# Performance work log

Measured on AMD Instinct MI355X. Metric: run time of the kernel, lower is better.

Reference implementation:

```python
import jax, jax.numpy as jnp
import numpy as np

# ---------- spherical offset pattern (setup-time, numpy, exact port) ----------

def _get_xy(dp, dt):
    t, c = np.tan, np.cos
    return np.array([
        [(-t(dt), 1/c(dt)*t(dp)), (0, t(dp)), (t(dt), 1/c(dt)*t(dp))],
        [(-t(dt), 0),             (1, 1),     (t(dt), 0)],
        [(-t(dt), -1/c(dt)*t(dp)), (0, -t(dp)), (t(dt), -1/c(dt)*t(dp))]])


def _cal_offset(h, w, r, c):
    phi = -((r + 0.5) / h * np.pi - np.pi / 2)
    theta = (c + 0.5) / w * 2 * np.pi - np.pi
    xys = _get_xy(np.pi / h, 2 * np.pi / w)
    x, y = xys[..., 0], xys[..., 1]
    rho = np.sqrt(x ** 2 + y ** 2)
    v = np.arctan(rho)
    new_phi = np.arcsin(np.cos(v) * np.sin(phi) + y * np.sin(v) * np.cos(phi) / rho)
    new_theta = theta + np.arctan(x * np.sin(v) / (rho * np.cos(phi) * np.cos(v) - y * np.sin(phi) * np.sin(v)))
    new_r = (-new_phi + np.pi / 2) * h / np.pi - 0.5
    new_c = (new_theta + np.pi) * w / 2 / np.pi - 0.5
    new_c = (new_c + w) % w
    res = np.stack([new_r, new_c], axis=-1)
    res[1, 1] = (r, c)
    for i in range(3):
        for j in range(3):
            res[i, j, 0] -= (r + i - 1)
            res[i, j, 1] -= (c + j - 1)
    return res.reshape(-1)  # (18,) ordered k=i*3+j, pairs (dy, dx)


def _offsets_map(h, w):
    with np.errstate(all='ignore'):
        co = np.array([[_cal_offset(h, w, i, j) for j in range(w)] for i in range(h)])
    return co.transpose(2, 0, 1)  # (18, h, w)


# ---------- jax forward ----------

def _bilinear_gather(x, py, px):
    # x: [B,C,H,W]; py/px: [K,H,W] float sample coords. Zero padding outside.
    B, C, H, W = x.shape
    y0 = jnp.floor(py); x0 = jnp.floor(px)
    wy = py - y0; wx = px - x0
    y0i = y0.astype(jnp.int32); x0i = x0.astype(jnp.int32)
    xf = x.reshape(B, C, H * W)

    def corner(yi, xi, wgt):
        valid = (yi >= 0) & (yi < H) & (xi >= 0) & (xi < W)
        idx = (jnp.clip(yi, 0, H - 1) * W + jnp.clip(xi, 0, W - 1)).reshape(-1)
        v = jnp.take(xf, idx, axis=2).reshape(B, C, *py.shape)  # [B,C,K,H,W]
        return v * (wgt * valid.astype(x.dtype))[None, None]

    return (corner(y0i,     x0i,     (1 - wy) * (1 - wx)) +
            corner(y0i,     x0i + 1, (1 - wy) * wx) +
            corner(y0i + 1, x0i,     wy * (1 - wx)) +
            corner(y0i + 1, x0i + 1, wy * wx))


def _forward(x, weight, bias, w_down, w_up, scale, offset):
    B, C, H, W = x.shape
    O = weight.shape[0]
    # frozen dense 3x3 conv (stride 1, pad 1)
    h = jax.lax.conv_general_dilated(
        x, weight, window_strides=(1, 1), padding=((1, 1), (1, 1)),
        dimension_numbers=('NCHW', 'OIHW', 'NCHW'))
    h = h + bias[None, :, None, None]
    # deform_conv2d with fixed spherical offsets (offset: [18,H,W] -> [9,2,H,W])
    off = offset.reshape(9, 2, H, W)
    dy, dx_ = off[:, 0], off[:, 1]
    kk = jnp.arange(9)
    ki = (kk // 3).astype(x.dtype); kj = (kk % 3).astype(x.dtype)
    pp = jnp.arange(H, dtype=x.dtype); qq = jnp.arange(W, dtype=x.dtype)
    py = pp[None, :, None] - 1.0 + ki[:, None, None] + dy  # [9,H,W]
    px = qq[None, None, :] - 1.0 + kj[:, None, None] + dx_
    sampled = _bilinear_gather(x, py, px)                   # [B,C,9,H,W]
    dconv = jnp.einsum('bckhw,ock->bohw', sampled, weight.reshape(O, C, 9))
    dconv = dconv + bias[None, :, None, None]
    # concat + dual 1x1 conv LoRA fusion + scaled residual
    cat = jnp.concatenate([dconv, h], axis=1)               # [B,2O,H,W]
    down = jnp.einsum('bchw,oc->bohw', cat, w_down)
    up = jnp.einsum('bchw,oc->bohw', down, w_up)
    return h + scale * up


def setup_inputs() -> dict:
    key = jax.random.key(0)
    ks = jax.random.split(key, 6)
    B, C, O, H, W = 4, 320, 320, 64, 64
    low = max(O // 1, 1)
    x = jax.random.normal(ks[0], (B, C, H, W), dtype=jnp.float32)
    weight = jax.random.normal(ks[1], (O, C, 3, 3), dtype=jnp.float32) * 0.02
    bias = jax.random.normal(ks[2], (O,), dtype=jnp.float32) * 0.02
    w_down = jax.random.normal(ks[3], (low, 2 * O), dtype=jnp.float32) * 0.02
    w_up = jax.random.normal(ks[4], (O, low), dtype=jnp.float32) * 0.02
    scale = jnp.asarray(1.0, dtype=jnp.float32)
    offset = jnp.asarray(_offsets_map(H, W), dtype=jnp.float32)  # [18,H,W]
    return {'x': x, 'weight': weight, 'bias': bias, 'w_down': w_down,
            'w_up': w_up, 'scale': scale, 'offset': offset}


def reference(x, weight, bias, w_down, w_up, scale, offset):
    return _forward(x, weight, bias, w_down, w_up, scale, offset)
```

## Files before the change

### kernel.cpp

```cpp
#include <hip/hip_runtime.h>
#include <stdint.h>


typedef __attribute__((ext_vector_type(4))) float f32x4;
typedef __attribute__((ext_vector_type(8))) short bf16x8;

typedef __attribute__((address_space(1))) const unsigned int uint_as1;
typedef __attribute__((address_space(3))) unsigned int uint_as3;

__device__ __forceinline__ void gl_lds16(const void* g, void* l) {
    __builtin_amdgcn_global_load_lds((uint_as1*)g, (uint_as3*)l, 16, 0, 0);
}

__device__ __forceinline__ unsigned short f2b(float f) {
    union { float f; uint32_t u; } v; v.f = f;
    uint32_t r = (v.u + 0x7FFFu + ((v.u >> 16) & 1u)) >> 16;
    return (unsigned short)r;
}
__device__ __forceinline__ float b2f(unsigned short h) {
    union { uint32_t u; float f; } v; v.u = ((uint32_t)h) << 16;
    return v.f;
}
__device__ __forceinline__ float b2f_lo(uint32_t u) {
    union { uint32_t u; float f; } v; v.u = u << 16;
    return v.f;
}
__device__ __forceinline__ float b2f_hi(uint32_t u) {
    union { uint32_t u; float f; } v; v.u = u & 0xFFFF0000u;
    return v.f;
}
__device__ __forceinline__ uint32_t pack2(float lo, float hi) {
    return (uint32_t)f2b(lo) | ((uint32_t)f2b(hi) << 16);
}

#define TAP8(AC, tv, wvx) \
    AC[0] += wvx * b2f_lo((uint32_t)tv.x); AC[1] += wvx * b2f_hi((uint32_t)tv.x); \
    AC[2] += wvx * b2f_lo((uint32_t)tv.y); AC[3] += wvx * b2f_hi((uint32_t)tv.y); \
    AC[4] += wvx * b2f_lo((uint32_t)tv.z); AC[5] += wvx * b2f_hi((uint32_t)tv.z); \
    AC[6] += wvx * b2f_lo((uint32_t)tv.w); AC[7] += wvx * b2f_hi((uint32_t)tv.w);

__global__ __launch_bounds__(256) void k_prep(const float* __restrict__ off,
                                              const float* __restrict__ w,
                                              const float* __restrict__ wd,
                                              const float* __restrict__ wu,
                                              uint32_t* __restrict__ oIdx,
                                              float* __restrict__ oW,
                                              unsigned short* __restrict__ Wr2,
                                              unsigned short* __restrict__ W2)
{
    const int bx = blockIdx.x, tid = threadIdx.x;
    if (bx < 144) {
        int gid = bx * 256 + tid;
        int k = gid >> 12;
        int p = gid & 4095;
        int i = p >> 6, j = p & 63;
        float dy = off[(2 * k) * 4096 + p];
        float dx = off[(2 * k + 1) * 4096 + p];
        float py = (float)(i - 1 + k / 3) + dy;
        float px = (float)(j - 1 + k % 3) + dx;
        float fy = floorf(py), fx = floorf(px);
        float wy = py - fy, wx = px - fx;
        fy = fminf(fmaxf(fy, -100.f), 100.f);
        fx = fminf(fmaxf(fx, -100.f), 100.f);
        int y0 = (int)fy, x0 = (int)fx;
        float vy0 = (y0 >= 0 && y0 < 64) ? 1.f : 0.f;
        float vy1 = (y0 >= -1 && y0 < 63) ? 1.f : 0.f;
        float vx0 = (x0 >= 0 && x0 < 64) ? 1.f : 0.f;
        float vx1 = (x0 >= -1 && x0 < 63) ? 1.f : 0.f;
        float w00 = (1.f - wy) * (1.f - wx) * vy0 * vx0;
        float w01 = (1.f - wy) * wx * vy0 * vx1;
        float w10 = wy * (1.f - wx) * vy1 * vx0;
        float w11 = wy * wx * vy1 * vx1;
        int ya = min(max(y0, 0), 63), yb = min(max(y0 + 1, 0), 63);
        int xa = min(max(x0, 0), 63), xb = min(max(x0 + 1, 0), 63);
        oIdx[gid * 2 + 0] = (uint32_t)(ya * 64 + xa) | ((uint32_t)(ya * 64 + xb) << 16);
        oIdx[gid * 2 + 1] = (uint32_t)(yb * 64 + xa) | ((uint32_t)(yb * 64 + xb) << 16);
        oW[gid * 4 + 0] = w00;
        oW[gid * 4 + 1] = w01;
        oW[gid * 4 + 2] = w10;
        oW[gid * 4 + 3] = w11;
    } else if (bx < 594) {
        int gid = (bx - 144) * 256 + tid;
        int cb = gid / 2880, m = gid - cb * 2880;
        int k = m / 320, o = m - k * 320;
        float v[8];
        #pragma unroll
        for (int cl = 0; cl < 8; ++cl) {
            int c = cb * 8 + cl;
            v[cl] = w[((size_t)o * 320 + c) * 9 + k];
        }
        int4 st;
        st.x = (int)pack2(v[0], v[1]);
        st.y = (int)pack2(v[2], v[3]);
        st.z = (int)pack2(v[4], v[5]);
        st.w = (int)pack2(v[6], v[7]);
        *(int4*)(Wr2 + (size_t)gid * 8) = st;
    } else {
        int gid = (bx - 594) * 256 + tid;
        int o = gid / 640, kk2 = gid % 640;
        float acc = 0.f;
        if (o < 320) {
            for (int l = 0; l < 320; ++l)
                acc += wu[o * 320 + l] * wd[l * 640 + kk2];
        }
        W2[(size_t)((kk2 >> 3) * 384 + o) * 8 + (kk2 & 7)] = f2b(acc);
    }
}

__global__ __launch_bounds__(256) void k_pack(const float* __restrict__ x,
                                              unsigned short* __restrict__ Xb)
{
    const int tid = threadIdx.x;
    const int sp = blockIdx.x, gl = blockIdx.y, b = blockIdx.z;
    const float* xb = x + ((size_t)b * 320 + gl * 8) * 4096;
    unsigned short* xpb = Xb + ((size_t)gl * 16384 + b * 4096) * 8;
    #pragma unroll
    for (int i = 0; i < 4; ++i) {
        int px = sp * 1024 + i * 256 + tid;
        float v0 = xb[0 * 4096 + px], v1 = xb[1 * 4096 + px];
        float v2 = xb[2 * 4096 + px], v3 = xb[3 * 4096 + px];
        float v4 = xb[4 * 4096 + px], v5 = xb[5 * 4096 + px];
        float v6 = xb[6 * 4096 + px], v7 = xb[7 * 4096 + px];
        int4 st;
        st.x = (int)pack2(v0, v1);
        st.y = (int)pack2(v2, v3);
        st.z = (int)pack2(v4, v5);
        st.w = (int)pack2(v6, v7);
        *(int4*)(xpb + (size_t)px * 8) = st;
    }
}

__global__ __launch_bounds__(256) void k_zgemm(const unsigned short* __restrict__ Xb,
                                               const unsigned short* __restrict__ Wr2,
                                               unsigned short* __restrict__ Z)
{
    __shared__ __align__(16) unsigned short As[2][8 * 160 * 8];
    __shared__ __align__(16) unsigned short Bs[2][8 * 128 * 8];
    const int tid = threadIdx.x;
    const int n0 = blockIdx.x * 128, m0 = blockIdx.y * 160;
    const int lane = tid & 63, w = tid >> 6;
    const int wm = w & 1, wn = w >> 1;
    const int quad = lane >> 4, nl = lane & 15;

#define STAGE(buf, s1) do { \
    _Pragma("unroll") \
    for (int q_ = 0; q_ < 5; ++q_) { \
        int u_ = tid + q_ * 256; \
        int kq_ = u_ / 160, m_ = u_ - kq_ * 160; \
        gl_lds16(Wr2 + ((size_t)(((s1) * 8 + kq_) * 2880 + m0 + m_)) * 8, &As[buf][u_ * 8]); \
    } \
    _Pragma("unroll") \
    for (int q_ = 0; q_ < 4; ++q_) { \
        int u_ = tid + q_ * 256; \
        int row_ = u_ >> 7, nn_ = n0 + (u_ & 127); \
        gl_lds16(Xb + ((size_t)((s1) * 8 + row_) * 16384 + nn_) * 8, &Bs[buf][u_ * 8]); \
    } \
} while (0)

    f32x4 acc[5][4];
    #pragma unroll
    for (int mt = 0; mt < 5; ++mt)
        #pragma unroll
        for (int nt = 0; nt < 4; ++nt)
            acc[mt][nt] = 0.f;

    STAGE(0, 0);
    asm volatile("s_waitcnt vmcnt(0)" ::: "memory");
    __builtin_amdgcn_s_barrier();
    __builtin_amdgcn_sched_barrier(0);

    for (int s = 0; s < 5; ++s) {
        const int p = s & 1, np = p ^ 1;
        if (s < 4) STAGE(np, s + 1);
        __builtin_amdgcn_sched_barrier(0);
        #pragma unroll
        for (int kc = 0; kc < 2; ++kc) {
            bf16x8 a[5], bf[4];
            #pragma unroll
            for (int mt = 0; mt < 5; ++mt)
                a[mt] = *(const bf16x8*)&As[p][((kc * 4 + quad) * 160 + wm * 80 + mt * 16 + nl) * 8];
            #pragma unroll
            for (int nt = 0; nt < 4; ++nt)
                bf[nt] = *(const bf16x8*)&Bs[p][((kc * 4 + quad) * 128 + wn * 64 + nt * 16 + nl) * 8];
            #pragma unroll
            for (int mt = 0; mt < 5; ++mt)
                #pragma unroll
                for (int nt = 0; nt < 4; ++nt)
                    acc[mt][nt] = __builtin_amdgcn_mfma_f32_16x16x32_bf16(a[mt], bf[nt], acc[mt][nt], 0, 0, 0);
        }
        asm volatile("s_waitcnt vmcnt(0)" ::: "memory");
        __builtin_amdgcn_s_barrier();
        __builtin_amdgcn_sched_barrier(0);
    }

    #pragma unroll
    for (int mt = 0; mt < 5; ++mt) {
        int o0m = m0 + wm * 80 + mt * 16 + quad * 4;
        #pragma unroll
        for (int nt = 0; nt < 4; ++nt) {
            int n2 = n0 + wn * 64 + nt * 16 + nl;
            unsigned short* pp = Z + ((size_t)(o0m >> 3) * 16384 + n2) * 8 + (o0m & 7);
            ushort4 st;
            st.x = f2b(acc[mt][nt][0]);
            st.y = f2b(acc[mt][nt][1]);
            st.z = f2b(acc[mt][nt][2]);
            st.w = f2b(acc[mt][nt][3]);
            *(ushort4*)pp = st;
        }
    }
#undef STAGE
}

__global__ __launch_bounds__(256) void k_blend(const unsigned short* __restrict__ Z,
                                               const uint32_t* __restrict__ oIdx,
                                               const float* __restrict__ oW,
                                               const float* __restrict__ bias,
                                               unsigned short* __restrict__ Cc)
{
    const int tid = threadIdx.x;
    const int px = blockIdx.x * 256 + tid;
    const int og0 = blockIdx.y * 4;
    const int b = blockIdx.z;
    const int r = px >> 6, c0 = px & 63;

    uint32_t i0[9], i1[9];
    float4 wv[9];
    int hidx[9];
    float hw[9];
    #pragma unroll
    for (int k = 0; k < 9; ++k) {
        int gi = (k << 12) + px;
        i0[k] = oIdx[gi * 2];
        i1[k] = oIdx[gi * 2 + 1];
        wv[k] = *(const float4*)&oW[(size_t)gi * 4];
        int rr = r + k / 3 - 1, cc = c0 + k % 3 - 1;
        bool valid = (rr >= 0) & (rr < 64) & (cc >= 0) & (cc < 64);
        hidx[k] = valid ? (rr * 64 + cc) : 0;
        hw[k] = valid ? 1.f : 0.f;
    }

    for (int oi = 0; oi < 4; ++oi) {
        int og = og0 + oi;
        float ac[8], ah[8];
        {
            float4 b0 = *(const float4*)&bias[og * 8];
            float4 b1 = *(const float4*)&bias[og * 8 + 4];
            ac[0] = b0.x; ac[1] = b0.y; ac[2] = b0.z; ac[3] = b0.w;
            ac[4] = b1.x; ac[5] = b1.y; ac[6] = b1.z; ac[7] = b1.w;
            #pragma unroll
            for (int j = 0; j < 8; ++j) ah[j] = ac[j];
        }
        #pragma unroll
        for (int k = 0; k < 9; ++k) {
            const unsigned short* Zb = Z + ((size_t)(k * 40 + og) * 16384 + b * 4096) * 8;
            int4 t0 = *(const int4*)(Zb + (size_t)(i0[k] & 0xFFFFu) * 8);
            int4 t1 = *(const int4*)(Zb + (size_t)(i0[k] >> 16) * 8);
            int4 t2 = *(const int4*)(Zb + (size_t)(i1[k] & 0xFFFFu) * 8);
            int4 t3 = *(const int4*)(Zb + (size_t)(i1[k] >> 16) * 8);
            int4 th = *(const int4*)(Zb + (size_t)hidx[k] * 8);
            TAP8(ac, t0, wv[k].x) TAP8(ac, t1, wv[k].y)
            TAP8(ac, t2, wv[k].z) TAP8(ac, t3, wv[k].w)
            TAP8(ah, th, hw[k])
        }
        int4 sd, sh;
        sd.x = (int)pack2(ac[0], ac[1]); sd.y = (int)pack2(ac[2], ac[3]);
        sd.z = (int)pack2(ac[4], ac[5]); sd.w = (int)pack2(ac[6], ac[7]);
        sh.x = (int)pack2(ah[0], ah[1]); sh.y = (int)pack2(ah[2], ah[3]);
        sh.z = (int)pack2(ah[4], ah[5]); sh.w = (int)pack2(ah[6], ah[7]);
        unsigned short* cp = Cc + ((size_t)og * 32768 + b * 4096 + px) * 8;
        *(int4*)cp = sd;
        *(int4*)(cp + 16384 * 8) = sh;
    }
}

__global__ __launch_bounds__(256) void k_final(const unsigned short* __restrict__ W2,
                                               const unsigned short* __restrict__ Cc,
                                               const float* __restrict__ scale,
                                               float* __restrict__ out)
{
    __shared__ __align__(16) unsigned short As[8 * 160 * 8];
    __shared__ __align__(16) unsigned short Bs[8 * 128 * 8];
    const int tid = threadIdx.x;
    const int n0 = blockIdx.x * 128, m0 = blockIdx.y * 160;
    const int lane = tid & 63, w = tid >> 6;
    const int wm = w & 1, wn = w >> 1;
    const int quad = lane >> 4, nl = lane & 15;
    f32x4 acc[5][4];
    #pragma unroll
    for (int mt = 0; mt < 5; ++mt)
        #pragma unroll
        for (int nt = 0; nt < 4; ++nt)
            acc[mt][nt] = 0.f;

    for (int s = 0; s < 10; ++s) {
        __syncthreads();
        #pragma unroll
        for (int q = 0; q < 5; ++q) {
            int u = tid + q * 256;
            int kq = u / 160, m = u - kq * 160;
            gl_lds16(W2 + ((size_t)(s * 8 + kq) * 384 + m0 + m) * 8, &As[u * 8]);
        }
        int h_off = (s < 5) ? 0 : 16384;
        int gq = (s < 5) ? s * 8 : (s - 5) * 8;
        #pragma unroll
        for (int q = 0; q < 4; ++q) {
            int u = tid + q * 256;
            int row = u >> 7, nn = n0 + (u & 127);
            gl_lds16(Cc + ((size_t)(gq + row) * 32768 + h_off + nn) * 8, &Bs[u * 8]);
        }
        __syncthreads();
        #pragma unroll
        for (int kc = 0; kc < 2; ++kc) {
            bf16x8 a[5], bf[4];
            #pragma unroll
            for (int mt = 0; mt < 5; ++mt)
                a[mt] = *(const bf16x8*)&As[((kc * 4 + quad) * 160 + wm * 80 + mt * 16 + nl) * 8];
            #pragma unroll
            for (int nt = 0; nt < 4; ++nt)
                bf[nt] = *(const bf16x8*)&Bs[((kc * 4 + quad) * 128 + wn * 64 + nt * 16 + nl) * 8];
            #pragma unroll
            for (int mt = 0; mt < 5; ++mt)
                #pragma unroll
                for (int nt = 0; nt < 4; ++nt)
                    acc[mt][nt] = __builtin_amdgcn_mfma_f32_16x16x32_bf16(a[mt], bf[nt], acc[mt][nt], 0, 0, 0);
        }
    }

    float sc = scale[0];
    #pragma unroll
    for (int mt = 0; mt < 5; ++mt) {
        int o0 = m0 + wm * 80 + mt * 16 + quad * 4;
        #pragma unroll
        for (int nt = 0; nt < 4; ++nt) {
            int n = n0 + wn * 64 + nt * 16 + nl;
            int b = n >> 12, px = n & 4095;
            ushort4 hv = *(const ushort4*)(Cc + ((size_t)(o0 >> 3) * 32768 + n + 16384) * 8 + (o0 & 7));
            size_t base = ((size_t)(b * 320 + o0)) * 4096 + px;
            out[base]            = b2f(hv.x) + sc * acc[mt][nt][0];
            out[base + 4096]     = b2f(hv.y) + sc * acc[mt][nt][1];
            out[base + 2 * 4096] = b2f(hv.z) + sc * acc[mt][nt][2];
            out[base + 3 * 4096] = b2f(hv.w) + sc * acc[mt][nt][3];
        }
    }
}

extern "C" void kernel_launch(void* const* d_in, const int* in_sizes, int n_in,
                              void* d_out, int out_size, void* d_ws, size_t ws_size,
                              hipStream_t stream)
{
    const float* x      = (const float*)d_in[0];
    const float* weight = (const float*)d_in[1];
    const float* bias   = (const float*)d_in[2];
    const float* w_down = (const float*)d_in[3];
    const float* w_up   = (const float*)d_in[4];
    const float* scale  = (const float*)d_in[5];
    const float* offset = (const float*)d_in[6];
    char* ws = (char*)d_ws;
    unsigned short* Cc    = (unsigned short*)(ws + 0);
    unsigned short* Wr2   = (unsigned short*)(ws + 25165824);
    unsigned short* W2    = (unsigned short*)(ws + 27377664);
    uint32_t*       oI    = (uint32_t*)(ws + 27869184);
    float*          oWt   = (float*)(ws + 28164096);
    unsigned short* Xb    = (unsigned short*)(ws + 28758016);
    unsigned short* Z     = (unsigned short*)(ws + 39909376);
    float* out = (float*)d_out;

    hipLaunchKernelGGL(k_prep, dim3(1554), dim3(256), 0, stream,
                       offset, weight, w_down, w_up, oI, oWt, Wr2, W2);
    hipLaunchKernelGGL(k_pack, dim3(4, 40, 4), dim3(256), 0, stream,
                       x, Xb);
    hipLaunchKernelGGL(k_zgemm, dim3(128, 18), dim3(256), 0, stream,
                       Xb, Wr2, Z);
    hipLaunchKernelGGL(k_blend, dim3(16, 10, 4), dim3(256), 0, stream,
                       Z, oI, oWt, bias, Cc);
    hipLaunchKernelGGL(k_final, dim3(128, 2), dim3(256), 0, stream,
                       W2, Cc, scale, out);
}
```

Measured before the change: 194.9 us.

## Fold pack into prep kernel, double-buffer final GEMM, halve its N tile

Merges the x bf16 packing into the prep kernel as extra blocks, removing one launch. The W2 weight-product loop uses vectorised float4 loads and four independent accumulators. The final LoRA GEMM now double-buffers its LDS tiles, prefetching the next K stage while the current one computes. Its N tile is halved to 64, doubling the grid to improve CU coverage, at the cost of less reuse of the A tile per block.

```diff
diff --git a/kernel.cpp b/kernel.cpp
--- a/kernel.cpp
+++ b/kernel.cpp
@@ -43,10 +43,12 @@
                                               const float* __restrict__ w,
                                               const float* __restrict__ wd,
                                               const float* __restrict__ wu,
+                                              const float* __restrict__ x,
                                               uint32_t* __restrict__ oIdx,
                                               float* __restrict__ oW,
                                               unsigned short* __restrict__ Wr2,
-                                              unsigned short* __restrict__ W2)
+                                              unsigned short* __restrict__ W2,
+                                              unsigned short* __restrict__ Xb)
 {
     const int bx = blockIdx.x, tid = threadIdx.x;
     if (bx < 144) {
@@ -95,38 +97,41 @@
         st.z = (int)pack2(v[4], v[5]);
         st.w = (int)pack2(v[6], v[7]);
         *(int4*)(Wr2 + (size_t)gid * 8) = st;
-    } else {
+    } else if (bx < 1554) {
         int gid = (bx - 594) * 256 + tid;
         int o = gid / 640, kk2 = gid % 640;
-        float acc = 0.f;
+        float a0 = 0.f, a1 = 0.f, a2 = 0.f, a3 = 0.f;
         if (o < 320) {
-            for (int l = 0; l < 320; ++l)
-                acc += wu[o * 320 + l] * wd[l * 640 + kk2];
-        }
-        W2[(size_t)((kk2 >> 3) * 384 + o) * 8 + (kk2 & 7)] = f2b(acc);
-    }
-}
-
-__global__ __launch_bounds__(256) void k_pack(const float* __restrict__ x,
-                                              unsigned short* __restrict__ Xb)
-{
-    const int tid = threadIdx.x;
-    const int sp = blockIdx.x, gl = blockIdx.y, b = blockIdx.z;
-    const float* xb = x + ((size_t)b * 320 + gl * 8) * 4096;
-    unsigned short* xpb = Xb + ((size_t)gl * 16384 + b * 4096) * 8;
-    #pragma unroll
-    for (int i = 0; i < 4; ++i) {
-        int px = sp * 1024 + i * 256 + tid;
-        float v0 = xb[0 * 4096 + px], v1 = xb[1 * 4096 + px];
-        float v2 = xb[2 * 4096 + px], v3 = xb[3 * 4096 + px];
-        float v4 = xb[4 * 4096 + px], v5 = xb[5 * 4096 + px];
-        float v6 = xb[6 * 4096 + px], v7 = xb[7 * 4096 + px];
-        int4 st;
-        st.x = (int)pack2(v0, v1);
-        st.y = (int)pack2(v2, v3);
-        st.z = (int)pack2(v4, v5);
-        st.w = (int)pack2(v6, v7);
-        *(int4*)(xpb + (size_t)px * 8) = st;
+            const float* wuo = wu + (size_t)o * 320;
+            for (int l = 0; l < 320; l += 4) {
+                float4 u4 = *(const float4*)(wuo + l);
+                a0 += u4.x * wd[(size_t)(l + 0) * 640 + kk2];
+                a1 += u4.y * wd[(size_t)(l + 1) * 640 + kk2];
+                a2 += u4.z * wd[(size_t)(l + 2) * 640 + kk2];
+                a3 += u4.w * wd[(size_t)(l + 3) * 640 + kk2];
+            }
+        }
+        W2[(size_t)((kk2 >> 3) * 384 + o) * 8 + (kk2 & 7)] = f2b((a0 + a1) + (a2 + a3));
+    } else {
+        int bz = bx - 1554;
+        int sp = bz & 3, rest = bz >> 2;
+        int gl = rest % 40, b = rest / 40;
+        const float* xb = x + ((size_t)b * 320 + gl * 8) * 4096;
+        unsigned short* xpb = Xb + ((size_t)gl * 16384 + b * 4096) * 8;
+        #pragma unroll
+        for (int i = 0; i < 4; ++i) {
+            int px = sp * 1024 + i * 256 + tid;
+            float v0 = xb[0 * 4096 + px], v1 = xb[1 * 4096 + px];
+            float v2 = xb[2 * 4096 + px], v3 = xb[3 * 4096 + px];
+            float v4 = xb[4 * 4096 + px], v5 = xb[5 * 4096 + px];
+            float v6 = xb[6 * 4096 + px], v7 = xb[7 * 4096 + px];
+            int4 st;
+            st.x = (int)pack2(v0, v1);
+            st.y = (int)pack2(v2, v3);
+            st.z = (int)pack2(v4, v5);
+            st.w = (int)pack2(v6, v7);
+            *(int4*)(xpb + (size_t)px * 8) = st;
+        }
     }
 }
 
@@ -278,52 +283,67 @@
                                                const float* __restrict__ scale,
                                                float* __restrict__ out)
 {
-    __shared__ __align__(16) unsigned short As[8 * 160 * 8];
-    __shared__ __align__(16) unsigned short Bs[8 * 128 * 8];
+    __shared__ __align__(16) unsigned short As[2][8 * 160 * 8];
+    __shared__ __align__(16) unsigned short Bs[2][8 * 64 * 8];
     const int tid = threadIdx.x;
-    const int n0 = blockIdx.x * 128, m0 = blockIdx.y * 160;
+    const int n0 = blockIdx.x * 64, m0 = blockIdx.y * 160;
     const int lane = tid & 63, w = tid >> 6;
     const int wm = w & 1, wn = w >> 1;
     const int quad = lane >> 4, nl = lane & 15;
-    f32x4 acc[5][4];
+
+#define STAGEF(buf, s1) do { \
+    _Pragma("unroll") \
+    for (int q_ = 0; q_ < 5; ++q_) { \
+        int u_ = tid + q_ * 256; \
+        int kq_ = u_ / 160, m_ = u_ - kq_ * 160; \
+        gl_lds16(W2 + ((size_t)(((s1) * 8 + kq_) * 384 + m0 + m_)) * 8, &As[buf][u_ * 8]); \
+    } \
+    { \
+        int h_off_ = ((s1) < 5) ? 0 : 16384; \
+        int gq_ = ((s1) < 5) ? (s1) * 8 : ((s1) - 5) * 8; \
+        _Pragma("unroll") \
+        for (int q_ = 0; q_ < 2; ++q_) { \
+            int u_ = tid + q_ * 256; \
+            int row_ = u_ >> 6, nn_ = n0 + (u_ & 63); \
+            gl_lds16(Cc + ((size_t)(gq_ + row_) * 32768 + h_off_ + nn_) * 8, &Bs[buf][u_ * 8]); \
+        } \
+    } \
+} while (0)
+
+    f32x4 acc[5][2];
     #pragma unroll
     for (int mt = 0; mt < 5; ++mt)
         #pragma unroll
-        for (int nt = 0; nt < 4; ++nt)
+        for (int nt = 0; nt < 2; ++nt)
             acc[mt][nt] = 0.f;
 
+    STAGEF(0, 0);
+    asm volatile("s_waitcnt vmcnt(0)" ::: "memory");
+    __builtin_amdgcn_s_barrier();
+    __builtin_amdgcn_sched_barrier(0);
+
     for (int s = 0; s < 10; ++s) {
-        __syncthreads();
-        #pragma unroll
-        for (int q = 0; q < 5; ++q) {
-            int u = tid + q * 256;
-            int kq = u / 160, m = u - kq * 160;
-            gl_lds16(W2 + ((size_t)(s * 8 + kq) * 384 + m0 + m) * 8, &As[u * 8]);
-        }
-        int h_off = (s < 5) ? 0 : 16384;
-        int gq = (s < 5) ? s * 8 : (s - 5) * 8;
-        #pragma unroll
-        for (int q = 0; q < 4; ++q) {
-            int u = tid + q * 256;
-            int row = u >> 7, nn = n0 + (u & 127);
-            gl_lds16(Cc + ((size_t)(gq + row) * 32768 + h_off + nn) * 8, &Bs[u * 8]);
-        }
-        __syncthreads();
+        const int p = s & 1, np = p ^ 1;
+        if (s < 9) STAGEF(np, s + 1);
+        __builtin_amdgcn_sched_barrier(0);
         #pragma unroll
         for (int kc = 0; kc < 2; ++kc) {
-            bf16x8 a[5], bf[4];
+            bf16x8 a[5], bf[2];
             #pragma unroll
             for (int mt = 0; mt < 5; ++mt)
-                a[mt] = *(const bf16x8*)&As[((kc * 4 + quad) * 160 + wm * 80 + mt * 16 + nl) * 8];
-            #pragma unroll
-            for (int nt = 0; nt < 4; ++nt)
-                bf[nt] = *(const bf16x8*)&Bs[((kc * 4 + quad) * 128 + wn * 64 + nt * 16 + nl) * 8];
+                a[mt] = *(const bf16x8*)&As[p][((kc * 4 + quad) * 160 + wm * 80 + mt * 16 + nl) * 8];
+            #pragma unroll
+            for (int nt = 0; nt < 2; ++nt)
+                bf[nt] = *(const bf16x8*)&Bs[p][((kc * 4 + quad) * 64 + wn * 32 + nt * 16 + nl) * 8];
             #pragma unroll
             for (int mt = 0; mt < 5; ++mt)
                 #pragma unroll
-                for (int nt = 0; nt < 4; ++nt)
+                for (int nt = 0; nt < 2; ++nt)
                     acc[mt][nt] = __builtin_amdgcn_mfma_f32_16x16x32_bf16(a[mt], bf[nt], acc[mt][nt], 0, 0, 0);
         }
+        asm volatile("s_waitcnt vmcnt(0)" ::: "memory");
+        __builtin_amdgcn_s_barrier();
+        __builtin_amdgcn_sched_barrier(0);
     }
 
     float sc = scale[0];
@@ -331,8 +351,8 @@
     for (int mt = 0; mt < 5; ++mt) {
         int o0 = m0 + wm * 80 + mt * 16 + quad * 4;
         #pragma unroll
-        for (int nt = 0; nt < 4; ++nt) {
-            int n = n0 + wn * 64 + nt * 16 + nl;
+        for (int nt = 0; nt < 2; ++nt) {
+            int n = n0 + wn * 32 + nt * 16 + nl;
             int b = n >> 12, px = n & 4095;
             ushort4 hv = *(const ushort4*)(Cc + ((size_t)(o0 >> 3) * 32768 + n + 16384) * 8 + (o0 & 7));
             size_t base = ((size_t)(b * 320 + o0)) * 4096 + px;
@@ -342,6 +362,7 @@
             out[base + 3 * 4096] = b2f(hv.w) + sc * acc[mt][nt][3];
         }
     }
+#undef STAGEF
 }
 
 extern "C" void kernel_launch(void* const* d_in, const int* in_sizes, int n_in,
@@ -365,14 +386,12 @@
     unsigned short* Z     = (unsigned short*)(ws + 39909376);
     float* out = (float*)d_out;
 
-    hipLaunchKernelGGL(k_prep, dim3(1554), dim3(256), 0, stream,
-                       offset, weight, w_down, w_up, oI, oWt, Wr2, W2);
-    hipLaunchKernelGGL(k_pack, dim3(4, 40, 4), dim3(256), 0, stream,
-                       x, Xb);
+    hipLaunchKernelGGL(k_prep, dim3(2194), dim3(256), 0, stream,
+                       offset, weight, w_down, w_up, x, oI, oWt, Wr2, W2, Xb);
     hipLaunchKernelGGL(k_zgemm, dim3(128, 18), dim3(256), 0, stream,
                        Xb, Wr2, Z);
     hipLaunchKernelGGL(k_blend, dim3(16, 10, 4), dim3(256), 0, stream,
                        Z, oI, oWt, bias, Cc);
-    hipLaunchKernelGGL(k_final, dim3(128, 2), dim3(256), 0, stream,
+    hipLaunchKernelGGL(k_final, dim3(256, 2), dim3(256), 0, stream,
                        W2, Cc, scale, out);
 }
```

Result: faster. 189.4 us (-2.8%).
